# Optimization experiments

Hardware: AMD Instinct MI355X
Metric: run time of the kernel (lower is better)

Reference implementation:

```python
import jax, jax.numpy as jnp
import numpy as np

DIM = 1024
HEADS = 16
HEAD_DIM = DIM // HEADS
SEQ_TGT = 2048  # query length
SEQ_SRC = 1024  # key/value length
BATCH = 4
LN_EPS = 1e-5


def setup_inputs() -> dict:
    key = jax.random.key(0)
    ks = jax.random.split(key, 8)
    s = 1.0 / np.sqrt(DIM)
    return {
        "q": jax.random.normal(ks[0], (BATCH, SEQ_TGT, DIM), dtype=jnp.float32),
        "kv": jax.random.normal(ks[1], (BATCH, SEQ_SRC, DIM), dtype=jnp.float32),
        "Wq": jax.random.normal(ks[2], (DIM, DIM), dtype=jnp.float32) * s,
        "Wk": jax.random.normal(ks[3], (DIM, DIM), dtype=jnp.float32) * s,
        "Wv": jax.random.normal(ks[4], (DIM, DIM), dtype=jnp.float32) * s,
        "Wo": jax.random.normal(ks[5], (DIM, DIM), dtype=jnp.float32) * s,
        "bo": jnp.zeros((DIM,), dtype=jnp.float32),
        "ln_g": jnp.ones((DIM,), dtype=jnp.float32),
        "ln_b": jnp.zeros((DIM,), dtype=jnp.float32),
    }


def _split_heads(x):
    b, n, _ = x.shape
    return x.reshape(b, n, HEADS, HEAD_DIM).transpose(0, 2, 1, 3)  # b h n d


def reference(q, kv, Wq, Wk, Wv, Wo, bo, ln_g, ln_b):
    # QKV projections (torch Linear: x @ W.T, no bias)
    qh = _split_heads(q @ Wq.T)    # [b,h,Nq,d]
    kh = _split_heads(kv @ Wk.T)   # [b,h,Nk,d]
    vh = _split_heads(kv @ Wv.T)   # [b,h,Nk,d]

    scale = HEAD_DIM ** -0.5
    qk = jnp.einsum('bhid,bhjd->bhij', qh, kh) * scale  # [b,h,Nq,Nk]

    # Block-causal mask: base [Nk,Nk] causal mask repeat_interleaved along query
    # axis by downscaling = Nq // Nk. Equivalent to allow iff (i // downscaling) >= j.
    downscaling = SEQ_TGT // SEQ_SRC  # = 2, upscaled_dim = 0
    i = jnp.arange(SEQ_TGT)[:, None]
    j = jnp.arange(SEQ_SRC)[None, :]
    neg_inf = jnp.asarray(-jnp.inf, dtype=qk.dtype)
    mask = jnp.where((i // downscaling) >= j, jnp.asarray(0.0, qk.dtype), neg_inf)

    attn = jax.nn.softmax(qk + mask[None, None, :, :], axis=-1)
    out = jnp.einsum('bhij,bhjd->bhid', attn, vh)           # [b,h,Nq,d]
    out = out.transpose(0, 2, 1, 3).reshape(BATCH, SEQ_TGT, DIM)

    # LayerNorm (norm_out=True)
    mu = jnp.mean(out, axis=-1, keepdims=True)
    var = jnp.mean(jnp.square(out - mu), axis=-1, keepdims=True)
    out = (out - mu) * jax.lax.rsqrt(var + LN_EPS) * ln_g + ln_b

    # Output projection (dropout is identity in eval mode)
    return out @ Wo.T + bo
```

## Files before the change

kernel.cpp:

```cpp
#include <hip/hip_runtime.h>

typedef unsigned short u16;
typedef unsigned int   u32;

typedef __bf16 bf16x8 __attribute__((ext_vector_type(8)));
typedef __bf16 bf16x4 __attribute__((ext_vector_type(4)));
typedef float  f32x4  __attribute__((ext_vector_type(4)));

__device__ __forceinline__ float bf2f(u16 v) {
    u32 u = ((u32)v) << 16; float f; __builtin_memcpy(&f, &u, 4); return f;
}
__device__ __forceinline__ u16 f2bf(float f) {
    __bf16 h = (__bf16)f; u16 r; __builtin_memcpy(&r, &h, 2); return r;
}

__device__ __forceinline__ void gload_lds16(const void* g, void* l) {
    __builtin_amdgcn_global_load_lds(
        (const __attribute__((address_space(1))) u32*)g,
        (__attribute__((address_space(3))) u32*)l, 16, 0, 0);
}

__device__ __forceinline__ void barrier_raw() {
    __builtin_amdgcn_s_barrier();
    asm volatile("" ::: "memory");
}

#define QSCALE 0.1803368801111204f

__global__ __launch_bounds__(256) void cvt_all(
    const float* __restrict__ q, const float* __restrict__ kv,
    const float* __restrict__ Wq, const float* __restrict__ Wk,
    const float* __restrict__ Wv, const float* __restrict__ Wo,
    u16* __restrict__ dst)
{
    const int total = 16 << 18;
    int i = blockIdx.x * 256 + threadIdx.x;
    const int stride = gridDim.x * 256;
    for (; i < total; i += stride) {
        int seg = i >> 18;
        const float* s; int off;
        if (seg < 8)        { s = q;  off = i; }
        else if (seg < 12)  { s = kv; off = i - (8 << 18); }
        else if (seg == 12) { s = Wq; off = i & 262143; }
        else if (seg == 13) { s = Wk; off = i & 262143; }
        else if (seg == 14) { s = Wv; off = i & 262143; }
        else                { s = Wo; off = i & 262143; }
        float4 v = reinterpret_cast<const float4*>(s)[off];
        ushort4 o;
        o.x = f2bf(v.x); o.y = f2bf(v.y); o.z = f2bf(v.z); o.w = f2bf(v.w);
        reinterpret_cast<ushort4*>(dst)[i] = o;
    }
}

template<int KK, int MH, bool RB>
__device__ __forceinline__ void qkv_phase(
    const char* ldsb, int d, int ha, int hb, int rbB, int fr, int fq,
    bf16x8 (&bF)[4], f32x4 (&acc)[8][4])
{
    const int sw = ((KK * 4 + fq) ^ (fr & 7)) * 16;
    if (RB) {
        #pragma unroll
        for (int ni = 0; ni < 4; ni++)
            bF[ni] = *reinterpret_cast<const bf16x8*>(
                ldsb + 65536 + d * 32768 + hb * 16384 + (rbB + ni * 16 + fr) * 128 + sw);
    }
    bf16x8 aF[4];
    #pragma unroll
    for (int j = 0; j < 4; j++)
        aF[j] = *reinterpret_cast<const bf16x8*>(
            ldsb + d * 32768 + ha * 16384 + ((MH * 4 + j) * 16 + fr) * 128 + sw);
    __builtin_amdgcn_s_setprio(1);
    #pragma unroll
    for (int j = 0; j < 4; j++)
        #pragma unroll
        for (int ni = 0; ni < 4; ni++)
            acc[MH * 4 + j][ni] = __builtin_amdgcn_mfma_f32_16x16x32_bf16(
                aF[j], bF[ni], acc[MH * 4 + j][ni], 0, 0, 0);
    __builtin_amdgcn_s_setprio(0);
}

__global__ __launch_bounds__(512, 2) void gemm_qkv8(
    const u16* __restrict__ q8, const u16* __restrict__ kv8,
    const u16* __restrict__ Wq8, const u16* __restrict__ Wk8,
    const u16* __restrict__ Wv8,
    u16* __restrict__ Qb, u16* __restrict__ Kb, u16* __restrict__ Vb)
{
    __shared__ __align__(16) u16 lds[65536];
    char* ldsb = (char*)lds;

    const int tid = threadIdx.x;
    const int l = tid & 63, w = tid >> 6;
    const int fr = l & 15, fq = l >> 4;

    const int bid = (int)blockIdx.x;
    const int lbid = (bid & 7) * 32 + (bid >> 3);
    const u16 *A, *W; u16* C; float scale = 1.0f; int rt, ct;
    if (lbid < 128)      { A = q8;  W = Wq8; C = Qb; scale = QSCALE; rt = lbid >> 2; ct = lbid & 3; }
    else if (lbid < 192) { int t = lbid - 128; A = kv8; W = Wk8; C = Kb; rt = t >> 2; ct = t & 3; }
    else                 { int t = lbid - 192; A = kv8; W = Wv8; C = Vb; rt = t >> 2; ct = t & 3; }
    const int brow = rt * 256, bcol = ct * 256;

    const int wr = (w >> 2) * 128, wc = (w & 3) * 64;
    const int ha = w >> 2;
    const int hb = (w & 3) >> 1;
    const int rbB = wc & 64;

    const int srow = l >> 3;
    const int sslot = (l & 7) ^ srow;

    const u16* srcA[2][2];
    const u16* srcB[2][2];
    #pragma unroll
    for (int h = 0; h < 2; h++)
        #pragma unroll
        for (int i = 0; i < 2; i++) {
            int grow = h * 128 + (2 * w + i) * 8 + srow;
            srcA[h][i] = A + (size_t)(brow + grow) * 1024 + sslot * 8;
            srcB[h][i] = W + (size_t)(bcol + grow) * 1024 + sslot * 8;
        }

    auto stageA = [&](int kt, int d) {
        #pragma unroll
        for (int h = 0; h < 2; h++)
            #pragma unroll
            for (int i = 0; i < 2; i++)
                gload_lds16(srcA[h][i] + kt * 64,
                            ldsb + d * 32768 + h * 16384 + (2 * w + i) * 1024);
    };
    auto stageBh = [&](int kt, int d, int h) {
        #pragma unroll
        for (int i = 0; i < 2; i++)
            gload_lds16(srcB[h][i] + kt * 64,
                        ldsb + 65536 + d * 32768 + h * 16384 + (2 * w + i) * 1024);
    };

    f32x4 acc[8][4] = {};

    stageA(0, 0); stageBh(0, 0, 0); stageBh(0, 0, 1);
    asm volatile("s_waitcnt vmcnt(0)" ::: "memory");
    barrier_raw();

    for (int kt = 0; kt < 16; ++kt) {
        const int d = kt & 1, nd = d ^ 1;
        const bool pre = (kt < 15);
        bf16x8 bF[4];

        if (pre) stageA(kt + 1, nd);
        qkv_phase<0, 0, true >(ldsb, d, ha, hb, rbB, fr, fq, bF, acc);
        barrier_raw();
        if (pre) stageBh(kt + 1, nd, 0);
        qkv_phase<0, 1, false>(ldsb, d, ha, hb, rbB, fr, fq, bF, acc);
        barrier_raw();
        if (pre) stageBh(kt + 1, nd, 1);
        qkv_phase<1, 0, true >(ldsb, d, ha, hb, rbB, fr, fq, bF, acc);
        barrier_raw();
        qkv_phase<1, 1, false>(ldsb, d, ha, hb, rbB, fr, fq, bF, acc);
        asm volatile("s_waitcnt vmcnt(0)" ::: "memory");
        barrier_raw();
    }

    #pragma unroll
    for (int mi = 0; mi < 8; mi++) {
        int row = brow + wr + mi * 16 + fq * 4;
        #pragma unroll
        for (int ni = 0; ni < 4; ni++) {
            int col = bcol + wc + ni * 16 + fr;
            #pragma unroll
            for (int r = 0; r < 4; r++)
                C[(size_t)(row + r) * 1024 + col] = f2bf(acc[mi][ni][r] * scale);
        }
    }
}

__global__ __launch_bounds__(512, 1) void gemm_out8(
    const u16* __restrict__ A, const u16* __restrict__ W,
    const float* __restrict__ bias, float* __restrict__ C)
{
    __shared__ __align__(16) u16 lds[49152];
    char* ldsb = (char*)lds;

    const int tid = threadIdx.x;
    const int l = tid & 63, w = tid >> 6;
    const int fr = l & 15, fq = l >> 4;

    const int bid = (int)blockIdx.x;
    const int lbid = (bid & 7) * 32 + (bid >> 3);
    const int rt = lbid >> 2, ct = lbid & 3;
    const int brow = rt * 128, bcol = ct * 256;

    const int wr = (w >> 2) * 64, wc = (w & 3) * 64;
    const int hb = (w & 3) >> 1;
    const int rbB = wc & 64;

    const int srow = l >> 3;
    const int sslot = (l & 7) ^ srow;

    const u16* srcA[2];
    const u16* srcB[2][2];
    #pragma unroll
    for (int i = 0; i < 2; i++) {
        int grow = (2 * w + i) * 8 + srow;
        srcA[i] = A + (size_t)(brow + grow) * 1024 + sslot * 8;
    }
    #pragma unroll
    for (int h = 0; h < 2; h++)
        #pragma unroll
        for (int i = 0; i < 2; i++) {
            int grow = h * 128 + (2 * w + i) * 8 + srow;
            srcB[h][i] = W + (size_t)(bcol + grow) * 1024 + sslot * 8;
        }

    auto stageA = [&](int kt, int d) {
        #pragma unroll
        for (int i = 0; i < 2; i++)
            gload_lds16(srcA[i] + kt * 64, ldsb + d * 16384 + (2 * w + i) * 1024);
    };
    auto stageB = [&](int kt, int d) {
        #pragma unroll
        for (int h = 0; h < 2; h++)
            #pragma unroll
            for (int i = 0; i < 2; i++)
                gload_lds16(srcB[h][i] + kt * 64,
                            ldsb + 32768 + d * 32768 + h * 16384 + (2 * w + i) * 1024);
    };

    f32x4 acc[4][4] = {};

    stageA(0, 0); stageB(0, 0);
    asm volatile("s_waitcnt vmcnt(0)" ::: "memory");
    barrier_raw();

    for (int kt = 0; kt < 16; ++kt) {
        const int d = kt & 1, nd = d ^ 1;
        const bool pre = (kt < 15);

        if (pre) stageA(kt + 1, nd);
        #pragma unroll
        for (int kk = 0; kk < 2; kk++) {
            const int sw = ((kk * 4 + fq) ^ (fr & 7)) * 16;
            bf16x8 aF[4], bF[4];
            #pragma unroll
            for (int j = 0; j < 4; j++)
                aF[j] = *reinterpret_cast<const bf16x8*>(
                    ldsb + d * 16384 + ((wr + j * 16 + fr) & 127) * 128 + sw);
            #pragma unroll
            for (int ni = 0; ni < 4; ni++)
                bF[ni] = *reinterpret_cast<const bf16x8*>(
                    ldsb + 32768 + d * 32768 + hb * 16384
                    + (rbB + ni * 16 + fr) * 128 + sw);
            __builtin_amdgcn_s_setprio(1);
            #pragma unroll
            for (int j = 0; j < 4; j++)
                #pragma unroll
                for (int ni = 0; ni < 4; ni++)
                    acc[j][ni] = __builtin_amdgcn_mfma_f32_16x16x32_bf16(
                        aF[j], bF[ni], acc[j][ni], 0, 0, 0);
            __builtin_amdgcn_s_setprio(0);
            if (kk == 0) {
                barrier_raw();
                if (pre) stageB(kt + 1, nd);
            }
        }
        asm volatile("s_waitcnt vmcnt(0)" ::: "memory");
        barrier_raw();
    }

    #pragma unroll
    for (int mi = 0; mi < 4; mi++) {
        int row = brow + wr + mi * 16 + fq * 4;
        #pragma unroll
        for (int ni = 0; ni < 4; ni++) {
            int col = bcol + wc + ni * 16 + fr;
            float bv = bias[col];
            #pragma unroll
            for (int r = 0; r < 4; r++)
                C[(size_t)(row + r) * 1024 + col] = acc[mi][ni][r] + bv;
        }
    }
}

__global__ __launch_bounds__(256) void attn_kernel(
    const u16* __restrict__ Q, const u16* __restrict__ K,
    const u16* __restrict__ V, u16* __restrict__ O)
{
    __shared__ __align__(16) u16 smem[25600];
    u16* Ks = smem;
    u16* Vt = smem + 8192;
    u16* Ps = smem + 16384;
    float* Ow = (float*)smem;

    const int tid = threadIdx.x;
    const int l = tid & 63, w = tid >> 6;
    const int fr = l & 15, fq = l >> 4;
    const int bh = blockIdx.y, b = bh >> 4, h = bh & 15;
    const int kp = tid & 31, d0 = (tid >> 5) * 8;
    const int kr = l >> 3, ksw = l & 7;
    u16* Pw = Ps + w * (32 * 72);

    const u16* Kbh = K + (size_t)b * 1024 * 1024 + h * 64;
    const u16* Vbh = V + (size_t)b * 1024 * 1024 + h * 64;

    bf16x8 ones;
    #pragma unroll
    for (int i = 0; i < 8; i++) ones[i] = (__bf16)1.0f;

    for (int half = 0; half < 2; ++half) {
        const int bq = half ? (int)blockIdx.x : 15 - (int)blockIdx.x;
        const int q0 = bq * 128;

        if (half) __syncthreads();

        bf16x8 qf[2][2];
        #pragma unroll
        for (int n = 0; n < 2; n++) {
            size_t qoff = (size_t)(b * 2048 + q0 + w * 32 + n * 16 + fr) * 1024 + h * 64;
            qf[n][0] = *reinterpret_cast<const bf16x8*>(Q + qoff + fq * 8);
            qf[n][1] = *reinterpret_cast<const bf16x8*>(Q + qoff + 32 + fq * 8);
        }

        float mx[2] = {-1e30f, -1e30f};
        f32x4 sumac[2] = {};
        f32x4 of[4][2] = {};

        {
            #pragma unroll
            for (int i = 0; i < 2; i++) {
                int cI = w * 2 + i;
                int r = cI * 8 + kr;
                gload_lds16(Kbh + (size_t)r * 1024 + ((ksw ^ (r & 7)) * 8), &Ks[cI * 512]);
            }
            const u16* vp = Vbh + (size_t)(2 * kp) * 1024 + d0;
            uint4 ra = *reinterpret_cast<const uint4*>(vp);
            uint4 rb = *reinterpret_cast<const uint4*>(vp + 1024);
            u16 ea[8], eb[8];
            __builtin_memcpy(ea, &ra, 16);
            __builtin_memcpy(eb, &rb, 16);
            #pragma unroll
            for (int jd = 0; jd < 8; jd++) {
                int d = d0 + jd;
                u32 pk = (u32)ea[jd] | ((u32)eb[jd] << 16);
                *(u32*)((char*)Vt + d * 128 + (((kp >> 2) ^ (d & 7)) * 16) + (kp & 3) * 4) = pk;
            }
        }
        __syncthreads();

        int cur = 0;
        for (int t = 0; t <= bq; ++t) {
            const bool pre = (t < bq);
            uint4 ra, rb;
            if (pre) {
                const int j0n = (t + 1) * 64;
                #pragma unroll
                for (int i = 0; i < 2; i++) {
                    int cI = w * 2 + i;
                    int r = cI * 8 + kr;
                    gload_lds16(Kbh + (size_t)(j0n + r) * 1024 + ((ksw ^ (r & 7)) * 8),
                                &Ks[(cur ^ 1) * 4096 + cI * 512]);
                }
                const u16* vp = Vbh + (size_t)(j0n + 2 * kp) * 1024 + d0;
                ra = *reinterpret_cast<const uint4*>(vp);
                rb = *reinterpret_cast<const uint4*>(vp + 1024);
            }

            f32x4 sf[4][2] = {};
            #pragma unroll
            for (int kk = 0; kk < 2; kk++) {
                bf16x8 kf[4];
                #pragma unroll
                for (int m = 0; m < 4; m++) {
                    int key = m * 16 + fr;
                    kf[m] = *reinterpret_cast<const bf16x8*>(
                        (char*)Ks + cur * 8192 + key * 128 + (((kk * 4 + fq) ^ (key & 7)) * 16));
                }
                #pragma unroll
                for (int m = 0; m < 4; m++)
                    #pragma unroll
                    for (int n = 0; n < 2; n++)
                        sf[m][n] = __builtin_amdgcn_mfma_f32_16x16x32_bf16(
                            kf[m], qf[n][kk], sf[m][n], 0, 0, 0);
            }

            const bool diag = (t == bq);
            float tmax[2] = {-1e30f, -1e30f};
            #pragma unroll
            for (int m = 0; m < 4; m++)
                #pragma unroll
                for (int n = 0; n < 2; n++)
                    #pragma unroll
                    for (int r = 0; r < 4; r++) {
                        float s = sf[m][n][r];
                        if (diag) {
                            int kl = m * 16 + fq * 4 + r;
                            int ql = w * 32 + n * 16 + fr;
                            if (kl > (ql >> 1)) s = -1e30f;
                        }
                        sf[m][n][r] = s;
                        tmax[n] = fmaxf(tmax[n], s);
                    }
            #pragma unroll
            for (int n = 0; n < 2; n++) {
                tmax[n] = fmaxf(tmax[n], __shfl_xor(tmax[n], 16));
                tmax[n] = fmaxf(tmax[n], __shfl_xor(tmax[n], 32));
            }

            const bool skip = __all(fmaxf(tmax[0] - mx[0], tmax[1] - mx[1]) <= 8.0f);
            if (!skip) {
                float al[2];
                #pragma unroll
                for (int n = 0; n < 2; n++) {
                    float mn = fmaxf(mx[n], tmax[n]);
                    al[n] = __builtin_amdgcn_exp2f(mx[n] - mn);
                    mx[n] = mn;
                    sumac[n] *= al[n];
                }
                #pragma unroll
                for (int m = 0; m < 4; m++)
                    #pragma unroll
                    for (int n = 0; n < 2; n++)
                        of[m][n] *= al[n];
            }

            #pragma unroll
            for (int m = 0; m < 4; m++)
                #pragma unroll
                for (int n = 0; n < 2; n++)
                    #pragma unroll
                    for (int r = 0; r < 4; r++)
                        sf[m][n][r] = __builtin_amdgcn_exp2f(sf[m][n][r] - mx[n]);

            #pragma unroll
            for (int m = 0; m < 4; m++)
                #pragma unroll
                for (int n = 0; n < 2; n++) {
                    bf16x4 pk;
                    pk[0] = (__bf16)sf[m][n][0]; pk[1] = (__bf16)sf[m][n][1];
                    pk[2] = (__bf16)sf[m][n][2]; pk[3] = (__bf16)sf[m][n][3];
                    int q = n * 16 + fr;
                    *(bf16x4*)((char*)Pw + q * 144 + m * 32 + fq * 8) = pk;
                }

            #pragma unroll
            for (int kk = 0; kk < 2; kk++) {
                bf16x8 pf[2], vf[4];
                #pragma unroll
                for (int n = 0; n < 2; n++) {
                    int q = n * 16 + fr;
                    pf[n] = *reinterpret_cast<const bf16x8*>(
                        (char*)Pw + q * 144 + kk * 64 + fq * 16);
                }
                #pragma unroll
                for (int m = 0; m < 4; m++) {
                    int d = m * 16 + fr;
                    vf[m] = *reinterpret_cast<const bf16x8*>(
                        (char*)Vt + cur * 8192 + d * 128 + (((kk * 4 + fq) ^ (d & 7)) * 16));
                }
                #pragma unroll
                for (int m = 0; m < 4; m++)
                    #pragma unroll
                    for (int n = 0; n < 2; n++)
                        of[m][n] = __builtin_amdgcn_mfma_f32_16x16x32_bf16(
                            vf[m], pf[n], of[m][n], 0, 0, 0);
                #pragma unroll
                for (int n = 0; n < 2; n++)
                    sumac[n] = __builtin_amdgcn_mfma_f32_16x16x32_bf16(
                        ones, pf[n], sumac[n], 0, 0, 0);
            }

            if (pre) {
                u16 ea[8], eb[8];
                __builtin_memcpy(ea, &ra, 16);
                __builtin_memcpy(eb, &rb, 16);
                #pragma unroll
                for (int jd = 0; jd < 8; jd++) {
                    int d = d0 + jd;
                    u32 pk = (u32)ea[jd] | ((u32)eb[jd] << 16);
                    *(u32*)((char*)Vt + (cur ^ 1) * 8192 + d * 128
                            + (((kp >> 2) ^ (d & 7)) * 16) + (kp & 3) * 4) = pk;
                }
            }
            __syncthreads();
            cur ^= 1;
        }

        float* OwW = Ow + w * (32 * 68);
        #pragma unroll
        for (int m = 0; m < 4; m++)
            #pragma unroll
            for (int n = 0; n < 2; n++) {
                f32x4 v = of[m][n] * (1.0f / sumac[n][0]);
                int q = n * 16 + fr;
                *reinterpret_cast<f32x4*>(&OwW[q * 68 + m * 16 + fq * 4]) = v;
            }
        {
            int ql = l >> 1, dh = l & 1;
            size_t grow = (size_t)(b * 2048 + q0 + w * 32 + ql) * 1024 + h * 64 + dh * 32;
            #pragma unroll
            for (int p = 0; p < 4; p++) {
                f32x4 a = *reinterpret_cast<const f32x4*>(&OwW[ql * 68 + dh * 32 + p * 8]);
                f32x4 c = *reinterpret_cast<const f32x4*>(&OwW[ql * 68 + dh * 32 + p * 8 + 4]);
                bf16x8 pk;
                pk[0]=(__bf16)a[0]; pk[1]=(__bf16)a[1]; pk[2]=(__bf16)a[2]; pk[3]=(__bf16)a[3];
                pk[4]=(__bf16)c[0]; pk[5]=(__bf16)c[1]; pk[6]=(__bf16)c[2]; pk[7]=(__bf16)c[3];
                *reinterpret_cast<bf16x8*>(O + grow + p * 8) = pk;
            }
        }
    }
}

__global__ __launch_bounds__(256) void ln_kernel(
    u16* __restrict__ buf, const float* __restrict__ g, const float* __restrict__ beta)
{
    const int row = blockIdx.x, tid = threadIdx.x;
    const size_t base = (size_t)row * 1024;
    ushort4 v = *reinterpret_cast<const ushort4*>(&buf[base + tid * 4]);
    float x0 = bf2f(v.x), x1 = bf2f(v.y), x2 = bf2f(v.z), x3 = bf2f(v.w);
    float s = x0 + x1 + x2 + x3;
    float q = x0 * x0 + x1 * x1 + x2 * x2 + x3 * x3;
    #pragma unroll
    for (int d = 32; d; d >>= 1) { s += __shfl_xor(s, d); q += __shfl_xor(q, d); }
    __shared__ float sm[8];
    int w = tid >> 6, l = tid & 63;
    if (l == 0) { sm[w] = s; sm[4 + w] = q; }
    __syncthreads();
    s = sm[0] + sm[1] + sm[2] + sm[3];
    q = sm[4] + sm[5] + sm[6] + sm[7];
    float mean = s * (1.0f / 1024.0f);
    float var = q * (1.0f / 1024.0f) - mean * mean;
    float rstd = rsqrtf(var + 1e-5f);
    float4 gv = *reinterpret_cast<const float4*>(&g[tid * 4]);
    float4 bv = *reinterpret_cast<const float4*>(&beta[tid * 4]);
    ushort4 o;
    o.x = f2bf((x0 - mean) * rstd * gv.x + bv.x);
    o.y = f2bf((x1 - mean) * rstd * gv.y + bv.y);
    o.z = f2bf((x2 - mean) * rstd * gv.z + bv.z);
    o.w = f2bf((x3 - mean) * rstd * gv.w + bv.w);
    *reinterpret_cast<ushort4*>(&buf[base + tid * 4]) = o;
}

extern "C" void kernel_launch(void* const* d_in, const int* in_sizes, int n_in,
                              void* d_out, int out_size, void* d_ws, size_t ws_size,
                              hipStream_t stream)
{
    const float* q    = (const float*)d_in[0];
    const float* kv   = (const float*)d_in[1];
    const float* Wq   = (const float*)d_in[2];
    const float* Wk   = (const float*)d_in[3];
    const float* Wv   = (const float*)d_in[4];
    const float* Wo   = (const float*)d_in[5];
    const float* bo   = (const float*)d_in[6];
    const float* ln_g = (const float*)d_in[7];
    const float* ln_b = (const float*)d_in[8];

    const size_t MQ = (size_t)8192 * 1024;
    const size_t MK = (size_t)4096 * 1024;
    const size_t MW = (size_t)1024 * 1024;

    u16* q8  = (u16*)d_ws;
    u16* kv8 = q8 + MQ;
    u16* Wq8 = kv8 + MK;
    u16* Wk8 = Wq8 + MW;
    u16* Wv8 = Wk8 + MW;
    u16* Wo8 = Wv8 + MW;
    u16* Qb  = Wo8 + MW;
    u16* Kb  = Qb + MQ;
    u16* Vb  = Kb + MK;
    u16* Ab  = Vb + MK;

    cvt_all<<<2048, 256, 0, stream>>>(q, kv, Wq, Wk, Wv, Wo, q8);
    gemm_qkv8<<<256, 512, 0, stream>>>(q8, kv8, Wq8, Wk8, Wv8, Qb, Kb, Vb);
    attn_kernel<<<dim3(8, 64), 256, 0, stream>>>(Qb, Kb, Vb, Ab);
    ln_kernel<<<8192, 256, 0, stream>>>(Ab, ln_g, ln_b);
    gemm_out8<<<256, 512, 0, stream>>>(Ab, Wo8, bo, (float*)d_out);
}
```

Before: 127.3 us.

## Process both causal query chunks concurrently with 512-thread attention blocks sharing K/V tiles

The attention kernel used to walk its two paired query chunks (a heavy and a light one) one after the other in a 256-thread block. It now runs them at the same time in a 512-thread block: waves 0-3 take the heavy chunk and waves 4-7 the light one, and both read the same double-buffered K/V tiles, so each tile is loaded once instead of twice. The K loads and the V transposing loads are split between the two wave groups, and block indices are interleaved to even out the load. The light-chunk waves sit idle at barriers once their causal range ends, and the larger LDS and thread count may lower occupancy.

```diff
diff --git a/kernel.cpp b/kernel.cpp
--- a/kernel.cpp
+++ b/kernel.cpp
@@ -279,11 +279,11 @@
     }
 }
 
-__global__ __launch_bounds__(256) void attn_kernel(
+__global__ __launch_bounds__(512, 4) void attn_kernel(
     const u16* __restrict__ Q, const u16* __restrict__ K,
     const u16* __restrict__ V, u16* __restrict__ O)
 {
-    __shared__ __align__(16) u16 smem[25600];
+    __shared__ __align__(16) u16 smem[34816];
     u16* Ks = smem;
     u16* Vt = smem + 8192;
     u16* Ps = smem + 16384;
@@ -293,216 +293,229 @@
     const int l = tid & 63, w = tid >> 6;
     const int fr = l & 15, fq = l >> 4;
     const int bh = blockIdx.y, b = bh >> 4, h = bh & 15;
-    const int kp = tid & 31, d0 = (tid >> 5) * 8;
     const int kr = l >> 3, ksw = l & 7;
+    const bool isH = (w < 4);
+    const int wl = w & 3;
     u16* Pw = Ps + w * (32 * 72);
+
+    const int t2 = tid & 255;
+    const int kp = t2 & 31, d0 = (t2 >> 5) * 8;
 
     const u16* Kbh = K + (size_t)b * 1024 * 1024 + h * 64;
     const u16* Vbh = V + (size_t)b * 1024 * 1024 + h * 64;
 
+    const int bidx = (int)blockIdx.x;
+    const int x = (bidx & 1) ? 7 - (bidx >> 1) : (bidx >> 1);
+    const int chunk = isH ? 15 - x : x;
+    const int q0 = chunk * 128;
+    const int T = 15 - x;
+
     bf16x8 ones;
     #pragma unroll
     for (int i = 0; i < 8; i++) ones[i] = (__bf16)1.0f;
 
-    for (int half = 0; half < 2; ++half) {
-        const int bq = half ? (int)blockIdx.x : 15 - (int)blockIdx.x;
-        const int q0 = bq * 128;
-
-        if (half) __syncthreads();
-
-        bf16x8 qf[2][2];
+    bf16x8 qf[2][2];
+    #pragma unroll
+    for (int n = 0; n < 2; n++) {
+        size_t qoff = (size_t)(b * 2048 + q0 + wl * 32 + n * 16 + fr) * 1024 + h * 64;
+        qf[n][0] = *reinterpret_cast<const bf16x8*>(Q + qoff + fq * 8);
+        qf[n][1] = *reinterpret_cast<const bf16x8*>(Q + qoff + 32 + fq * 8);
+    }
+
+    float mx[2] = {-1e30f, -1e30f};
+    f32x4 sumac[2] = {};
+    f32x4 of[4][2] = {};
+
+    auto process = [&](int cur, bool diag) {
+        f32x4 sf[4][2] = {};
+        #pragma unroll
+        for (int kk = 0; kk < 2; kk++) {
+            bf16x8 kf[4];
+            #pragma unroll
+            for (int m = 0; m < 4; m++) {
+                int key = m * 16 + fr;
+                kf[m] = *reinterpret_cast<const bf16x8*>(
+                    (char*)Ks + cur * 8192 + key * 128 + (((kk * 4 + fq) ^ (key & 7)) * 16));
+            }
+            #pragma unroll
+            for (int m = 0; m < 4; m++)
+                #pragma unroll
+                for (int n = 0; n < 2; n++)
+                    sf[m][n] = __builtin_amdgcn_mfma_f32_16x16x32_bf16(
+                        kf[m], qf[n][kk], sf[m][n], 0, 0, 0);
+        }
+
+        float tmax[2] = {-1e30f, -1e30f};
+        #pragma unroll
+        for (int m = 0; m < 4; m++)
+            #pragma unroll
+            for (int n = 0; n < 2; n++)
+                #pragma unroll
+                for (int r = 0; r < 4; r++) {
+                    float s = sf[m][n][r];
+                    if (diag) {
+                        int kl = m * 16 + fq * 4 + r;
+                        int ql = wl * 32 + n * 16 + fr;
+                        if (kl > (ql >> 1)) s = -1e30f;
+                    }
+                    sf[m][n][r] = s;
+                    tmax[n] = fmaxf(tmax[n], s);
+                }
         #pragma unroll
         for (int n = 0; n < 2; n++) {
-            size_t qoff = (size_t)(b * 2048 + q0 + w * 32 + n * 16 + fr) * 1024 + h * 64;
-            qf[n][0] = *reinterpret_cast<const bf16x8*>(Q + qoff + fq * 8);
-            qf[n][1] = *reinterpret_cast<const bf16x8*>(Q + qoff + 32 + fq * 8);
-        }
-
-        float mx[2] = {-1e30f, -1e30f};
-        f32x4 sumac[2] = {};
-        f32x4 of[4][2] = {};
-
-        {
-            #pragma unroll
-            for (int i = 0; i < 2; i++) {
-                int cI = w * 2 + i;
-                int r = cI * 8 + kr;
-                gload_lds16(Kbh + (size_t)r * 1024 + ((ksw ^ (r & 7)) * 8), &Ks[cI * 512]);
-            }
-            const u16* vp = Vbh + (size_t)(2 * kp) * 1024 + d0;
-            uint4 ra = *reinterpret_cast<const uint4*>(vp);
-            uint4 rb = *reinterpret_cast<const uint4*>(vp + 1024);
-            u16 ea[8], eb[8];
-            __builtin_memcpy(ea, &ra, 16);
-            __builtin_memcpy(eb, &rb, 16);
-            #pragma unroll
-            for (int jd = 0; jd < 8; jd++) {
-                int d = d0 + jd;
-                u32 pk = (u32)ea[jd] | ((u32)eb[jd] << 16);
-                *(u32*)((char*)Vt + d * 128 + (((kp >> 2) ^ (d & 7)) * 16) + (kp & 3) * 4) = pk;
-            }
-        }
-        __syncthreads();
-
-        int cur = 0;
-        for (int t = 0; t <= bq; ++t) {
-            const bool pre = (t < bq);
-            uint4 ra, rb;
-            if (pre) {
-                const int j0n = (t + 1) * 64;
+            tmax[n] = fmaxf(tmax[n], __shfl_xor(tmax[n], 16));
+            tmax[n] = fmaxf(tmax[n], __shfl_xor(tmax[n], 32));
+        }
+
+        const bool skip = __all(fmaxf(tmax[0] - mx[0], tmax[1] - mx[1]) <= 8.0f);
+        if (!skip) {
+            float al[2];
+            #pragma unroll
+            for (int n = 0; n < 2; n++) {
+                float mn = fmaxf(mx[n], tmax[n]);
+                al[n] = __builtin_amdgcn_exp2f(mx[n] - mn);
+                mx[n] = mn;
+                sumac[n] *= al[n];
+            }
+            #pragma unroll
+            for (int m = 0; m < 4; m++)
+                #pragma unroll
+                for (int n = 0; n < 2; n++)
+                    of[m][n] *= al[n];
+        }
+
+        #pragma unroll
+        for (int m = 0; m < 4; m++)
+            #pragma unroll
+            for (int n = 0; n < 2; n++)
+                #pragma unroll
+                for (int r = 0; r < 4; r++)
+                    sf[m][n][r] = __builtin_amdgcn_exp2f(sf[m][n][r] - mx[n]);
+
+        #pragma unroll
+        for (int m = 0; m < 4; m++)
+            #pragma unroll
+            for (int n = 0; n < 2; n++) {
+                bf16x4 pk;
+                pk[0] = (__bf16)sf[m][n][0]; pk[1] = (__bf16)sf[m][n][1];
+                pk[2] = (__bf16)sf[m][n][2]; pk[3] = (__bf16)sf[m][n][3];
+                int q = n * 16 + fr;
+                *(bf16x4*)((char*)Pw + q * 144 + m * 32 + fq * 8) = pk;
+            }
+
+        #pragma unroll
+        for (int kk = 0; kk < 2; kk++) {
+            bf16x8 pf[2], vf[4];
+            #pragma unroll
+            for (int n = 0; n < 2; n++) {
+                int q = n * 16 + fr;
+                pf[n] = *reinterpret_cast<const bf16x8*>(
+                    (char*)Pw + q * 144 + kk * 64 + fq * 16);
+            }
+            #pragma unroll
+            for (int m = 0; m < 4; m++) {
+                int d = m * 16 + fr;
+                vf[m] = *reinterpret_cast<const bf16x8*>(
+                    (char*)Vt + cur * 8192 + d * 128 + (((kk * 4 + fq) ^ (d & 7)) * 16));
+            }
+            #pragma unroll
+            for (int m = 0; m < 4; m++)
+                #pragma unroll
+                for (int n = 0; n < 2; n++)
+                    of[m][n] = __builtin_amdgcn_mfma_f32_16x16x32_bf16(
+                        vf[m], pf[n], of[m][n], 0, 0, 0);
+            #pragma unroll
+            for (int n = 0; n < 2; n++)
+                sumac[n] = __builtin_amdgcn_mfma_f32_16x16x32_bf16(
+                    ones, pf[n], sumac[n], 0, 0, 0);
+        }
+    };
+
+    if (isH) {
+        #pragma unroll
+        for (int i = 0; i < 2; i++) {
+            int cI = wl * 2 + i;
+            int r = cI * 8 + kr;
+            gload_lds16(Kbh + (size_t)r * 1024 + ((ksw ^ (r & 7)) * 8), &Ks[cI * 512]);
+        }
+    } else {
+        const u16* vp = Vbh + (size_t)(2 * kp) * 1024 + d0;
+        uint4 ra = *reinterpret_cast<const uint4*>(vp);
+        uint4 rb = *reinterpret_cast<const uint4*>(vp + 1024);
+        u16 ea[8], eb[8];
+        __builtin_memcpy(ea, &ra, 16);
+        __builtin_memcpy(eb, &rb, 16);
+        #pragma unroll
+        for (int jd = 0; jd < 8; jd++) {
+            int d = d0 + jd;
+            u32 pk = (u32)ea[jd] | ((u32)eb[jd] << 16);
+            *(u32*)((char*)Vt + d * 128 + (((kp >> 2) ^ (d & 7)) * 16) + (kp & 3) * 4) = pk;
+        }
+    }
+    __syncthreads();
+
+    int cur = 0;
+    for (int t = 0; t <= T; ++t) {
+        const bool pre = (t < T);
+        uint4 ra, rb;
+        if (pre) {
+            const int j0n = (t + 1) * 64;
+            if (isH) {
                 #pragma unroll
                 for (int i = 0; i < 2; i++) {
-                    int cI = w * 2 + i;
+                    int cI = wl * 2 + i;
                     int r = cI * 8 + kr;
                     gload_lds16(Kbh + (size_t)(j0n + r) * 1024 + ((ksw ^ (r & 7)) * 8),
                                 &Ks[(cur ^ 1) * 4096 + cI * 512]);
                 }
+            } else {
                 const u16* vp = Vbh + (size_t)(j0n + 2 * kp) * 1024 + d0;
                 ra = *reinterpret_cast<const uint4*>(vp);
                 rb = *reinterpret_cast<const uint4*>(vp + 1024);
             }
-
-            f32x4 sf[4][2] = {};
-            #pragma unroll
-            for (int kk = 0; kk < 2; kk++) {
-                bf16x8 kf[4];
-                #pragma unroll
-                for (int m = 0; m < 4; m++) {
-                    int key = m * 16 + fr;
-                    kf[m] = *reinterpret_cast<const bf16x8*>(
-                        (char*)Ks + cur * 8192 + key * 128 + (((kk * 4 + fq) ^ (key & 7)) * 16));
-                }
-                #pragma unroll
-                for (int m = 0; m < 4; m++)
-                    #pragma unroll
-                    for (int n = 0; n < 2; n++)
-                        sf[m][n] = __builtin_amdgcn_mfma_f32_16x16x32_bf16(
-                            kf[m], qf[n][kk], sf[m][n], 0, 0, 0);
-            }
-
-            const bool diag = (t == bq);
-            float tmax[2] = {-1e30f, -1e30f};
-            #pragma unroll
-            for (int m = 0; m < 4; m++)
-                #pragma unroll
-                for (int n = 0; n < 2; n++)
-                    #pragma unroll
-                    for (int r = 0; r < 4; r++) {
-                        float s = sf[m][n][r];
-                        if (diag) {
-                            int kl = m * 16 + fq * 4 + r;
-                            int ql = w * 32 + n * 16 + fr;
-                            if (kl > (ql >> 1)) s = -1e30f;
-                        }
-                        sf[m][n][r] = s;
-                        tmax[n] = fmaxf(tmax[n], s);
-                    }
-            #pragma unroll
-            for (int n = 0; n < 2; n++) {
-                tmax[n] = fmaxf(tmax[n], __shfl_xor(tmax[n], 16));
-                tmax[n] = fmaxf(tmax[n], __shfl_xor(tmax[n], 32));
-            }
-
-            const bool skip = __all(fmaxf(tmax[0] - mx[0], tmax[1] - mx[1]) <= 8.0f);
-            if (!skip) {
-                float al[2];
-                #pragma unroll
-                for (int n = 0; n < 2; n++) {
-                    float mn = fmaxf(mx[n], tmax[n]);
-                    al[n] = __builtin_amdgcn_exp2f(mx[n] - mn);
-                    mx[n] = mn;
-                    sumac[n] *= al[n];
-                }
-                #pragma unroll
-                for (int m = 0; m < 4; m++)
-                    #pragma unroll
-                    for (int n = 0; n < 2; n++)
-                        of[m][n] *= al[n];
-            }
-
-            #pragma unroll
-            for (int m = 0; m < 4; m++)
-                #pragma unroll
-                for (int n = 0; n < 2; n++)
-                    #pragma unroll
-                    for (int r = 0; r < 4; r++)
-                        sf[m][n][r] = __builtin_amdgcn_exp2f(sf[m][n][r] - mx[n]);
-
-            #pragma unroll
-            for (int m = 0; m < 4; m++)
-                #pragma unroll
-                for (int n = 0; n < 2; n++) {
-                    bf16x4 pk;
-                    pk[0] = (__bf16)sf[m][n][0]; pk[1] = (__bf16)sf[m][n][1];
-                    pk[2] = (__bf16)sf[m][n][2]; pk[3] = (__bf16)sf[m][n][3];
-                    int q = n * 16 + fr;
-                    *(bf16x4*)((char*)Pw + q * 144 + m * 32 + fq * 8) = pk;
-                }
-
-            #pragma unroll
-            for (int kk = 0; kk < 2; kk++) {
-                bf16x8 pf[2], vf[4];
-                #pragma unroll
-                for (int n = 0; n < 2; n++) {
-                    int q = n * 16 + fr;
-                    pf[n] = *reinterpret_cast<const bf16x8*>(
-                        (char*)Pw + q * 144 + kk * 64 + fq * 16);
-                }
-                #pragma unroll
-                for (int m = 0; m < 4; m++) {
-                    int d = m * 16 + fr;
-                    vf[m] = *reinterpret_cast<const bf16x8*>(
-                        (char*)Vt + cur * 8192 + d * 128 + (((kk * 4 + fq) ^ (d & 7)) * 16));
-                }
-                #pragma unroll
-                for (int m = 0; m < 4; m++)
-                    #pragma unroll
-                    for (int n = 0; n < 2; n++)
-                        of[m][n] = __builtin_amdgcn_mfma_f32_16x16x32_bf16(
-                            vf[m], pf[n], of[m][n], 0, 0, 0);
-                #pragma unroll
-                for (int n = 0; n < 2; n++)
-                    sumac[n] = __builtin_amdgcn_mfma_f32_16x16x32_bf16(
-                        ones, pf[n], sumac[n], 0, 0, 0);
-            }
-
-            if (pre) {
-                u16 ea[8], eb[8];
-                __builtin_memcpy(ea, &ra, 16);
-                __builtin_memcpy(eb, &rb, 16);
-                #pragma unroll
-                for (int jd = 0; jd < 8; jd++) {
-                    int d = d0 + jd;
-                    u32 pk = (u32)ea[jd] | ((u32)eb[jd] << 16);
-                    *(u32*)((char*)Vt + (cur ^ 1) * 8192 + d * 128
-                            + (((kp >> 2) ^ (d & 7)) * 16) + (kp & 3) * 4) = pk;
-                }
-            }
-            __syncthreads();
-            cur ^= 1;
-        }
-
-        float* OwW = Ow + w * (32 * 68);
-        #pragma unroll
-        for (int m = 0; m < 4; m++)
-            #pragma unroll
-            for (int n = 0; n < 2; n++) {
-                f32x4 v = of[m][n] * (1.0f / sumac[n][0]);
-                int q = n * 16 + fr;
-                *reinterpret_cast<f32x4*>(&OwW[q * 68 + m * 16 + fq * 4]) = v;
-            }
-        {
-            int ql = l >> 1, dh = l & 1;
-            size_t grow = (size_t)(b * 2048 + q0 + w * 32 + ql) * 1024 + h * 64 + dh * 32;
-            #pragma unroll
-            for (int p = 0; p < 4; p++) {
-                f32x4 a = *reinterpret_cast<const f32x4*>(&OwW[ql * 68 + dh * 32 + p * 8]);
-                f32x4 c = *reinterpret_cast<const f32x4*>(&OwW[ql * 68 + dh * 32 + p * 8 + 4]);
-                bf16x8 pk;
-                pk[0]=(__bf16)a[0]; pk[1]=(__bf16)a[1]; pk[2]=(__bf16)a[2]; pk[3]=(__bf16)a[3];
-                pk[4]=(__bf16)c[0]; pk[5]=(__bf16)c[1]; pk[6]=(__bf16)c[2]; pk[7]=(__bf16)c[3];
-                *reinterpret_cast<bf16x8*>(O + grow + p * 8) = pk;
-            }
+        }
+
+        if (isH)
+            process(cur, t == 15 - x);
+        else if (t <= x)
+            process(cur, t == x);
+
+        if (pre && !isH) {
+            u16 ea[8], eb[8];
+            __builtin_memcpy(ea, &ra, 16);
+            __builtin_memcpy(eb, &rb, 16);
+            #pragma unroll
+            for (int jd = 0; jd < 8; jd++) {
+                int d = d0 + jd;
+                u32 pk = (u32)ea[jd] | ((u32)eb[jd] << 16);
+                *(u32*)((char*)Vt + (cur ^ 1) * 8192 + d * 128
+                        + (((kp >> 2) ^ (d & 7)) * 16) + (kp & 3) * 4) = pk;
+            }
+        }
+        __syncthreads();
+        cur ^= 1;
+    }
+
+    float* OwW = Ow + w * (32 * 68);
+    #pragma unroll
+    for (int m = 0; m < 4; m++)
+        #pragma unroll
+        for (int n = 0; n < 2; n++) {
+            f32x4 v = of[m][n] * (1.0f / sumac[n][0]);
+            int q = n * 16 + fr;
+            *reinterpret_cast<f32x4*>(&OwW[q * 68 + m * 16 + fq * 4]) = v;
+        }
+    {
+        int ql = l >> 1, dh = l & 1;
+        size_t grow = (size_t)(b * 2048 + q0 + wl * 32 + ql) * 1024 + h * 64 + dh * 32;
+        #pragma unroll
+        for (int p = 0; p < 4; p++) {
+            f32x4 a = *reinterpret_cast<const f32x4*>(&OwW[ql * 68 + dh * 32 + p * 8]);
+            f32x4 c = *reinterpret_cast<const f32x4*>(&OwW[ql * 68 + dh * 32 + p * 8 + 4]);
+            bf16x8 pk;
+            pk[0]=(__bf16)a[0]; pk[1]=(__bf16)a[1]; pk[2]=(__bf16)a[2]; pk[3]=(__bf16)a[3];
+            pk[4]=(__bf16)c[0]; pk[5]=(__bf16)c[1]; pk[6]=(__bf16)c[2]; pk[7]=(__bf16)c[3];
+            *reinterpret_cast<bf16x8*>(O + grow + p * 8) = pk;
         }
     }
 }
@@ -568,7 +581,7 @@
 
     cvt_all<<<2048, 256, 0, stream>>>(q, kv, Wq, Wk, Wv, Wo, q8);
     gemm_qkv8<<<256, 512, 0, stream>>>(q8, kv8, Wq8, Wk8, Wv8, Qb, Kb, Vb);
-    attn_kernel<<<dim3(8, 64), 256, 0, stream>>>(Qb, Kb, Vb, Ab);
+    attn_kernel<<<dim3(8, 64), 512, 0, stream>>>(Qb, Kb, Vb, Ab);
     ln_kernel<<<8192, 256, 0, stream>>>(Ab, ln_g, ln_b);
     gemm_out8<<<256, 512, 0, stream>>>(Ab, Wo8, bo, (float*)d_out);
 }
```

After: 176.0 us. +38.2%, slower.

## Triple-buffer K tiles with two-ahead prefetch and partial vmcnt waits

Applied to the files above, without the earlier changes.

Grows shared memory so K has three LDS buffers and issues the async global-to-LDS K load two tiles ahead, while V stays double-buffered through registers. The full __syncthreads is replaced by an explicit s_waitcnt that leaves the two newest K loads in flight, followed by a raw barrier. The aim is to hide K load latency behind more compute. It costs extra LDS per block, which may reduce occupancy, and relies on hand-counted vmcnt values being correct.

```diff
diff --git a/kernel.cpp b/kernel.cpp
--- a/kernel.cpp
+++ b/kernel.cpp
@@ -283,10 +283,10 @@
     const u16* __restrict__ Q, const u16* __restrict__ K,
     const u16* __restrict__ V, u16* __restrict__ O)
 {
-    __shared__ __align__(16) u16 smem[25600];
+    __shared__ __align__(16) u16 smem[29696];
     u16* Ks = smem;
-    u16* Vt = smem + 8192;
-    u16* Ps = smem + 16384;
+    u16* Vt = smem + 12288;
+    u16* Ps = smem + 20480;
     float* Ow = (float*)smem;
 
     const int tid = threadIdx.x;
@@ -304,6 +304,28 @@
     #pragma unroll
     for (int i = 0; i < 8; i++) ones[i] = (__bf16)1.0f;
 
+    auto stageK = [&](int jt, int kb) {
+        #pragma unroll
+        for (int i = 0; i < 2; i++) {
+            int cI = w * 2 + i;
+            int r = cI * 8 + kr;
+            gload_lds16(Kbh + (size_t)(jt * 64 + r) * 1024 + ((ksw ^ (r & 7)) * 8),
+                        (char*)Ks + kb * 8192 + cI * 1024);
+        }
+    };
+    auto writeV = [&](uint4 ra, uint4 rb, int vb) {
+        u16 ea[8], eb[8];
+        __builtin_memcpy(ea, &ra, 16);
+        __builtin_memcpy(eb, &rb, 16);
+        #pragma unroll
+        for (int jd = 0; jd < 8; jd++) {
+            int d = d0 + jd;
+            u32 pk = (u32)ea[jd] | ((u32)eb[jd] << 16);
+            *(u32*)((char*)Vt + vb * 8192 + d * 128
+                    + (((kp >> 2) ^ (d & 7)) * 16) + (kp & 3) * 4) = pk;
+        }
+    };
+
     for (int half = 0; half < 2; ++half) {
         const int bq = half ? (int)blockIdx.x : 15 - (int)blockIdx.x;
         const int q0 = bq * 128;
@@ -323,44 +345,28 @@
         f32x4 of[4][2] = {};
 
         {
-            #pragma unroll
-            for (int i = 0; i < 2; i++) {
-                int cI = w * 2 + i;
-                int r = cI * 8 + kr;
-                gload_lds16(Kbh + (size_t)r * 1024 + ((ksw ^ (r & 7)) * 8), &Ks[cI * 512]);
-            }
             const u16* vp = Vbh + (size_t)(2 * kp) * 1024 + d0;
             uint4 ra = *reinterpret_cast<const uint4*>(vp);
             uint4 rb = *reinterpret_cast<const uint4*>(vp + 1024);
-            u16 ea[8], eb[8];
-            __builtin_memcpy(ea, &ra, 16);
-            __builtin_memcpy(eb, &rb, 16);
-            #pragma unroll
-            for (int jd = 0; jd < 8; jd++) {
-                int d = d0 + jd;
-                u32 pk = (u32)ea[jd] | ((u32)eb[jd] << 16);
-                *(u32*)((char*)Vt + d * 128 + (((kp >> 2) ^ (d & 7)) * 16) + (kp & 3) * 4) = pk;
-            }
-        }
-        __syncthreads();
-
-        int cur = 0;
+            stageK(0, 0);
+            if (bq >= 1) stageK(1, 1);
+            writeV(ra, rb, 0);
+            if (bq >= 1) asm volatile("s_waitcnt vmcnt(2) lgkmcnt(0)" ::: "memory");
+            else         asm volatile("s_waitcnt vmcnt(0) lgkmcnt(0)" ::: "memory");
+            barrier_raw();
+        }
+
         for (int t = 0; t <= bq; ++t) {
-            const bool pre = (t < bq);
+            const int kb = t % 3, vb = t & 1;
+            const bool preV = (t < bq);
+            const bool preK = (t + 2 <= bq);
             uint4 ra, rb;
-            if (pre) {
-                const int j0n = (t + 1) * 64;
-                #pragma unroll
-                for (int i = 0; i < 2; i++) {
-                    int cI = w * 2 + i;
-                    int r = cI * 8 + kr;
-                    gload_lds16(Kbh + (size_t)(j0n + r) * 1024 + ((ksw ^ (r & 7)) * 8),
-                                &Ks[(cur ^ 1) * 4096 + cI * 512]);
-                }
-                const u16* vp = Vbh + (size_t)(j0n + 2 * kp) * 1024 + d0;
+            if (preV) {
+                const u16* vp = Vbh + (size_t)((t + 1) * 64 + 2 * kp) * 1024 + d0;
                 ra = *reinterpret_cast<const uint4*>(vp);
                 rb = *reinterpret_cast<const uint4*>(vp + 1024);
             }
+            if (preK) stageK(t + 2, (t + 2) % 3);
 
             f32x4 sf[4][2] = {};
             #pragma unroll
@@ -370,7 +376,7 @@
                 for (int m = 0; m < 4; m++) {
                     int key = m * 16 + fr;
                     kf[m] = *reinterpret_cast<const bf16x8*>(
-                        (char*)Ks + cur * 8192 + key * 128 + (((kk * 4 + fq) ^ (key & 7)) * 16));
+                        (char*)Ks + kb * 8192 + key * 128 + (((kk * 4 + fq) ^ (key & 7)) * 16));
                 }
                 #pragma unroll
                 for (int m = 0; m < 4; m++)
@@ -452,7 +458,7 @@
                 for (int m = 0; m < 4; m++) {
                     int d = m * 16 + fr;
                     vf[m] = *reinterpret_cast<const bf16x8*>(
-                        (char*)Vt + cur * 8192 + d * 128 + (((kk * 4 + fq) ^ (d & 7)) * 16));
+                        (char*)Vt + vb * 8192 + d * 128 + (((kk * 4 + fq) ^ (d & 7)) * 16));
                 }
                 #pragma unroll
                 for (int m = 0; m < 4; m++)
@@ -466,20 +472,11 @@
                         ones, pf[n], sumac[n], 0, 0, 0);
             }
 
-            if (pre) {
-                u16 ea[8], eb[8];
-                __builtin_memcpy(ea, &ra, 16);
-                __builtin_memcpy(eb, &rb, 16);
-                #pragma unroll
-                for (int jd = 0; jd < 8; jd++) {
-                    int d = d0 + jd;
-                    u32 pk = (u32)ea[jd] | ((u32)eb[jd] << 16);
-                    *(u32*)((char*)Vt + (cur ^ 1) * 8192 + d * 128
-                            + (((kp >> 2) ^ (d & 7)) * 16) + (kp & 3) * 4) = pk;
-                }
-            }
-            __syncthreads();
-            cur ^= 1;
+            if (preV) writeV(ra, rb, vb ^ 1);
+
+            if (preK) asm volatile("s_waitcnt vmcnt(2) lgkmcnt(0)" ::: "memory");
+            else      asm volatile("s_waitcnt vmcnt(0) lgkmcnt(0)" ::: "memory");
+            barrier_raw();
         }
 
         float* OwW = Ow + w * (32 * 68);
```

After: 131.1 us. 1.03x slower.
